# Performance work log

Hardware: AMD Instinct MI355X
Metric: run time of the kernel (lower is better)

The kernel has to match this reference:

```python
import jax, jax.numpy as jnp
import numpy as np

# bitsandbytes NF4 codebook (16 levels)
NF4 = jnp.array([-1.0, -0.6961928009986877, -0.5250730514526367, -0.39491748809814453,
                 -0.28444138169288635, -0.18477343022823334, -0.09105003625154495, 0.0,
                 0.07958029955625534, 0.16093020141124725, 0.24611230194568634,
                 0.33791524171829224, 0.44070982933044434, 0.5626170039176941,
                 0.7229568362236023, 1.0], dtype=jnp.float32)
BLOCK = 64  # NF4 quantization blocksize
HD, M, TOKENS = 4096, 11008, 512


def dequant_nf4(codes, absmax, out_f, in_f):
    # codes: int [out_f, in_f] in [0,16); absmax: float [out_f*in_f/BLOCK]
    w = NF4[codes.reshape(-1, BLOCK)] * absmax[:, None]
    return w.reshape(out_f, in_f)


def setup_inputs() -> dict:
    key = jax.random.key(0)
    ks = jax.random.split(key, 7)
    x = jax.random.normal(ks[0], (TOKENS, HD), dtype=jnp.float32)
    gate_codes = jax.random.randint(ks[1], (M, HD), 0, 16, dtype=jnp.int32)
    up_codes = jax.random.randint(ks[2], (M, HD), 0, 16, dtype=jnp.int32)
    down_codes = jax.random.randint(ks[3], (HD, M), 0, 16, dtype=jnp.int32)
    n_blk = (M * HD) // BLOCK
    gate_absmax = jax.random.uniform(ks[4], (n_blk,), dtype=jnp.float32) * 0.02 + 1e-3
    up_absmax = jax.random.uniform(ks[5], (n_blk,), dtype=jnp.float32) * 0.02 + 1e-3
    down_absmax = jax.random.uniform(ks[6], (n_blk,), dtype=jnp.float32) * 0.02 + 1e-3
    return {"x": x, "gate_codes": gate_codes, "gate_absmax": gate_absmax,
            "up_codes": up_codes, "up_absmax": up_absmax,
            "down_codes": down_codes, "down_absmax": down_absmax}


def reference(x, gate_codes, gate_absmax, up_codes, up_absmax, down_codes, down_absmax):
    # Dequantize NF4 weights on the fly, then SwiGLU MLP:
    # down( silu(gate(x)) * up(x) )
    Wg = dequant_nf4(gate_codes, gate_absmax, M, HD)   # [m, hd]
    Wu = dequant_nf4(up_codes, up_absmax, M, HD)       # [m, hd]
    Wd = dequant_nf4(down_codes, down_absmax, HD, M)   # [hd, m]
    g = x @ Wg.T                                       # [tokens, m]
    u = x @ Wu.T                                       # [tokens, m]
    h = jax.nn.silu(g) * u                             # [tokens, m]
    return h @ Wd.T                                    # [tokens, hd]
```

## Files before the change

### kernel.cpp

```cpp
#include <hip/hip_runtime.h>
#include <hip/hip_fp16.h>
#include <cstdint>
#include <cstddef>


using float4v = __attribute__((ext_vector_type(4))) float;
using half8   = __attribute__((ext_vector_type(8))) _Float16;

__constant__ float NF4TAB[16] = {
  -1.0f, -0.6961928009986877f, -0.5250730514526367f, -0.39491748809814453f,
  -0.28444138169288635f, -0.18477343022823334f, -0.09105003625154495f, 0.0f,
  0.07958029955625534f, 0.16093020141124725f, 0.24611230194568634f,
  0.33791524171829224f, 0.44070982933044434f, 0.5626170039176941f,
  0.7229568362236023f, 1.0f };


__global__ __launch_bounds__(256) void repack_kernel(
    const int* __restrict__ codes, const float* __restrict__ amax,
    unsigned char* __restrict__ outp, float* __restrict__ outam,
    int K, int Kb, int KbG)
{
  __shared__ unsigned char lds[4][32 * 36];
  const int tid  = threadIdx.x;
  const int lane = tid & 63;
  const int w    = tid >> 6;
  const int l15  = lane & 15;
  const int hi   = lane >> 4;

  const int bid  = blockIdx.x;
  const int tile = bid / KbG;
  const int kb   = (bid % KbG) * 4 + w;

  const int* src = codes + (size_t)tile * 32 * K + (size_t)kb * 64;

  #pragma unroll
  for (int i = 0; i < 8; ++i) {
    const int row = i * 4 + hi;
    const int4 c = *(const int4*)(src + (size_t)row * K + l15 * 4);
    const unsigned short v =
      (unsigned short)((c.x | (c.y << 4)) | ((c.z | (c.w << 4)) << 8));
    *(unsigned short*)&lds[w][row * 36 + l15 * 2] = v;
  }
  asm volatile("s_waitcnt lgkmcnt(0)" ::: "memory");
  __builtin_amdgcn_sched_barrier(0);

  uint4 o;
  o.x = *(const unsigned*)&lds[w][l15 * 36 + hi * 4];
  o.y = *(const unsigned*)&lds[w][l15 * 36 + 16 + hi * 4];
  o.z = *(const unsigned*)&lds[w][(l15 + 16) * 36 + hi * 4];
  o.w = *(const unsigned*)&lds[w][(l15 + 16) * 36 + 16 + hi * 4];
  *(uint4*)(outp + (((size_t)tile * Kb + kb) * 64 + lane) * 16) = o;

  if (lane < 32)
    outam[((size_t)tile * Kb + kb) * 32 + lane] =
      amax[(size_t)(tile * 32 + lane) * Kb + kb];
}

template <bool ATOMIC>
__global__ __launch_bounds__(256, 3) void gemm_nf4(
    const __half* __restrict__ Apk,
    const unsigned char* __restrict__ p0, const float* __restrict__ am0,
    const unsigned char* __restrict__ p1, const float* __restrict__ am1,
    __half* __restrict__ o0, __half* __restrict__ o1,
    float* __restrict__ outF,
    int N, int K, int Kc, int Ntiles)
{
  __shared__ unsigned ptab[256];

  const int tid  = threadIdx.x;
  const int lane = tid & 63;
  const int wave = tid >> 6;
  const int l15  = lane & 15;

  {
    __half2 pr = __floats2half2_rn(NF4TAB[tid & 15], NF4TAB[tid >> 4]);
    ptab[tid] = *(const unsigned*)&pr;
  }
  __syncthreads();

  int nt, r2;
  if (ATOMIC) {
    const int xcd  = blockIdx.x & 7;
    const int slot = blockIdx.x >> 3;
    r2 = xcd >> 1;
    nt = (xcd & 1) * (Ntiles >> 1) + slot;
  } else {
    const int nwg = gridDim.x;
    const int bid = (blockIdx.x & 7) * (nwg >> 3) + (blockIdx.x >> 3);
    nt = bid % Ntiles;
    r2 = bid / Ntiles;
  }

  const int k0 = ATOMIC ? r2 * Kc : 0;
  const int nk = Kc >> 6;
  const unsigned char* pk = (!ATOMIC && r2) ? p1 : p0;
  const float* amx        = (!ATOMIC && r2) ? am1 : am0;
  __half* outH            = (!ATOMIC && r2) ? o1 : o0;

  const int col0 = nt * 32;
  const int Kb   = K >> 6;
  const int kb0q = k0 >> 6;

  const uint4* pc  = (const uint4*)(pk + (((size_t)nt * Kb + kb0q) * 64 + lane) * 16);
  const float* pam = amx + ((size_t)nt * Kb + kb0q) * 32 + l15;

  const __half* pA = Apk + ((size_t)((k0 >> 5) * 32 + wave * 8)) * 512
                         + (size_t)lane * 8;

  float4v acc[8][2];
  {
    float4v z = {0.f, 0.f, 0.f, 0.f};
    #pragma unroll
    for (int i = 0; i < 8; ++i)
      #pragma unroll
      for (int j = 0; j < 2; ++j) acc[i][j] = z;
  }

  uint4 cq;
  float af[2];

#define LOADCQ()                                                                \
  { cq = *pc; af[0] = pam[0]; af[1] = pam[16];                                  \
    pc += 64; pam += 32; }

#define DEQD(DST, D, AM2)                                                       \
  { unsigned _w0 = ptab[(D) & 255];                                             \
    unsigned _w1 = ptab[((D) >> 8) & 255];                                      \
    unsigned _w2 = ptab[((D) >> 16) & 255];                                     \
    unsigned _w3 = ptab[(D) >> 24];                                             \
    __half2 _p0 = __hmul2(*(const __half2*)&_w0, AM2);                          \
    __half2 _p1 = __hmul2(*(const __half2*)&_w1, AM2);                          \
    __half2 _p2 = __hmul2(*(const __half2*)&_w2, AM2);                          \
    __half2 _p3 = __hmul2(*(const __half2*)&_w3, AM2);                          \
    uint4 _wv;                                                                  \
    _wv.x = *(const unsigned*)&_p0; _wv.y = *(const unsigned*)&_p1;             \
    _wv.z = *(const unsigned*)&_p2; _wv.w = *(const unsigned*)&_p3;             \
    DST = *(const half8*)&_wv; }

  LOADCQ();

  for (int kt = 0; kt < nk; ++kt) {
    const __half _a0 = __float2half(af[0]);
    const __half _a1 = __float2half(af[1]);
    const __half2 am20{_a0, _a0}, am21{_a1, _a1};
    half8 bq00, bq01, bq10, bq11;
    DEQD(bq00, cq.x, am20);
    DEQD(bq01, cq.y, am20);
    DEQD(bq10, cq.z, am21);
    DEQD(bq11, cq.w, am21);

    half8 ap[8];
    #pragma unroll
    for (int i = 0; i < 8; ++i)
      ap[i] = *(const half8*)(pA + i * 512);

    if (kt + 1 < nk) LOADCQ();

    #pragma unroll
    for (int i = 0; i < 8; ++i) {
      acc[i][0] = __builtin_amdgcn_mfma_f32_16x16x32_f16(ap[i], bq00, acc[i][0], 0, 0, 0);
      acc[i][1] = __builtin_amdgcn_mfma_f32_16x16x32_f16(ap[i], bq10, acc[i][1], 0, 0, 0);
    }

    #pragma unroll
    for (int i = 0; i < 8; ++i)
      ap[i] = *(const half8*)(pA + 16384 + i * 512);

    #pragma unroll
    for (int i = 0; i < 8; ++i) {
      acc[i][0] = __builtin_amdgcn_mfma_f32_16x16x32_f16(ap[i], bq01, acc[i][0], 0, 0, 0);
      acc[i][1] = __builtin_amdgcn_mfma_f32_16x16x32_f16(ap[i], bq11, acc[i][1], 0, 0, 0);
    }

    pA += 32768;
  }

  if (ATOMIC) {
    const int ccol0 = col0 + l15;
    const int crow0 = wave * 128 + ((lane >> 4) << 2);
    #pragma unroll
    for (int i = 0; i < 8; ++i)
      #pragma unroll
      for (int j = 0; j < 2; ++j)
        #pragma unroll
        for (int rr = 0; rr < 4; ++rr) {
          const size_t idx = (size_t)(crow0 + i * 16 + rr) * N + (ccol0 + j * 16);
          atomicAdd(&outF[idx], acc[i][j][rr]);
        }
  } else {
    const int jj    = lane & 7;
    const int lb    = (lane >> 3) & 1;
    const int rbase = (lane >> 4) << 2;
    const int kb    = col0 >> 5;
    #pragma unroll
    for (int i = 0; i < 8; ++i) {
      const int mb = wave * 8 + i;
      #pragma unroll
      for (int j = 0; j < 2; ++j) {
        const int lp = (j * 2 + lb) * 16 + rbase;
        #pragma unroll
        for (int rr = 0; rr < 4; ++rr) {
          const size_t a = ((size_t)(kb * 32 + mb) * 64 + (lp + rr)) * 8 + jj;
          outH[a] = __float2half(acc[i][j][rr]);
        }
      }
    }
  }
#undef LOADCQ
#undef DEQD
}

__global__ void cast_pack_kernel(const float* __restrict__ x,
                                 __half* __restrict__ xp, int nGrp) {
  int pid = blockIdx.x * blockDim.x + threadIdx.x;
  if (pid >= nGrp) return;
  const int lane = pid & 63;
  const int grp  = pid >> 6;
  const int mb   = grp & 31;
  const int kb   = grp >> 5;
  const int m = mb * 16 + (lane & 15);
  const int k = kb * 32 + ((lane >> 4) << 3);
  const float4* src = (const float4*)(x + (size_t)m * 4096 + k);
  float4 v0 = src[0], v1 = src[1];
  __half2 h0 = __floats2half2_rn(v0.x, v0.y), h1 = __floats2half2_rn(v0.z, v0.w);
  __half2 h2 = __floats2half2_rn(v1.x, v1.y), h3 = __floats2half2_rn(v1.z, v1.w);
  uint4 o;
  o.x = *(const unsigned*)&h0; o.y = *(const unsigned*)&h1;
  o.z = *(const unsigned*)&h2; o.w = *(const unsigned*)&h3;
  ((uint4*)xp)[pid] = o;
}

__global__ void swiglu_kernel(const __half* __restrict__ g,
                              const __half* __restrict__ u,
                              __half* __restrict__ h, int n2) {
  int i = blockIdx.x * blockDim.x + threadIdx.x;
  if (i < n2) {
    float2 gf = __half22float2(((const __half2*)g)[i]);
    float2 uf = __half22float2(((const __half2*)u)[i]);
    float h0 = gf.x / (1.f + __expf(-gf.x)) * uf.x;
    float h1 = gf.y / (1.f + __expf(-gf.y)) * uf.y;
    ((__half2*)h)[i] = __floats2half2_rn(h0, h1);
  }
}

extern "C" void kernel_launch(void* const* d_in, const int* in_sizes, int n_in,
                              void* d_out, int out_size, void* d_ws, size_t ws_size,
                              hipStream_t stream)
{
  (void)in_sizes; (void)n_in; (void)ws_size;
  const float* x            = (const float*)d_in[0];
  const int*   gate_codes   = (const int*)d_in[1];
  const float* gate_absmax  = (const float*)d_in[2];
  const int*   up_codes     = (const int*)d_in[3];
  const float* up_absmax    = (const float*)d_in[4];
  const int*   down_codes   = (const int*)d_in[5];
  const float* down_absmax  = (const float*)d_in[6];
  float* out = (float*)d_out;

  __half* xp = (__half*)d_ws;
  __half* g  = xp + (size_t)512 * 4096;
  __half* u  = g  + (size_t)512 * 11008;
  unsigned char* pg = (unsigned char*)(u + (size_t)512 * 11008);
  unsigned char* pu = pg + (size_t)344 * 64 * 1024;
  unsigned char* pd = pu + (size_t)344 * 64 * 1024;
  float* amg = (float*)(pd + (size_t)128 * 172 * 1024);
  float* amu = amg + (size_t)344 * 64 * 32;
  float* amd = amu + (size_t)344 * 64 * 32;

  hipMemsetAsync(d_out, 0, (size_t)out_size * sizeof(float), stream);

  cast_pack_kernel<<<1024, 256, 0, stream>>>(x, xp, (512 * 4096) / 8);

  repack_kernel<<<5504, 256, 0, stream>>>(gate_codes, gate_absmax, pg, amg,
                                          4096, 64, 16);
  repack_kernel<<<5504, 256, 0, stream>>>(up_codes, up_absmax, pu, amu,
                                          4096, 64, 16);
  repack_kernel<<<5504, 256, 0, stream>>>(down_codes, down_absmax, pd, amd,
                                          11008, 172, 43);

  gemm_nf4<false><<<688, 256, 0, stream>>>(xp, pg, amg, pu, amu,
                                           g, u, nullptr,
                                           11008, 4096, 4096, 344);

  swiglu_kernel<<<11008, 256, 0, stream>>>(g, u, g, (512 * 11008) / 2);

  gemm_nf4<true><<<512, 256, 0, stream>>>(g, pd, amd,
                                          nullptr, nullptr, nullptr, nullptr,
                                          out, 4096, 11008, 2752, 128);
}
```

Measured before the change: 810.9 us.

## Reshape NF4 GEMM tiles to 256x64 with 4x4 MFMA blocking and double-buffered codes

The GEMM workgroup tile changes from 512 rows by 32 columns to 256 rows by 64 columns. Each wave now holds a 4x4 grid of MFMA accumulators, so every A fragment is reused across four dequantized B fragments and fewer A loads are needed per MFMA. The repack kernel now writes a 64-column packed layout directly from registers with no LDS staging. The main loop is unrolled by two, with separate prefetch registers for the codes and absmax two steps ahead. In exchange, more dequantization work is done per wave for each A load, and register pressure may rise under the launch bound of 3.

New measurement: 705.3 us. 1.15x faster.

```diff
diff --git a/kernel.cpp b/kernel.cpp
--- a/kernel.cpp
+++ b/kernel.cpp
@@ -17,43 +17,47 @@
 
 __global__ __launch_bounds__(256) void repack_kernel(
     const int* __restrict__ codes, const float* __restrict__ amax,
-    unsigned char* __restrict__ outp, float* __restrict__ outam,
+    unsigned char* __restrict__ pb, float* __restrict__ pam,
     int K, int Kb, int KbG)
 {
-  __shared__ unsigned char lds[4][32 * 36];
   const int tid  = threadIdx.x;
   const int lane = tid & 63;
   const int w    = tid >> 6;
   const int l15  = lane & 15;
   const int hi   = lane >> 4;
 
-  const int bid  = blockIdx.x;
-  const int tile = bid / KbG;
-  const int kb   = (bid % KbG) * 4 + w;
-
-  const int* src = codes + (size_t)tile * 32 * K + (size_t)kb * 64;
-
+  const int tile = blockIdx.x / KbG;
+  const int kbg  = blockIdx.x % KbG;
+  const int kb   = kbg * 4 + w;
+
+  unsigned dk0[4], dk1[4];
   #pragma unroll
-  for (int i = 0; i < 8; ++i) {
-    const int row = i * 4 + hi;
-    const int4 c = *(const int4*)(src + (size_t)row * K + l15 * 4);
-    const unsigned short v =
-      (unsigned short)((c.x | (c.y << 4)) | ((c.z | (c.w << 4)) << 8));
-    *(unsigned short*)&lds[w][row * 36 + l15 * 2] = v;
-  }
-  asm volatile("s_waitcnt lgkmcnt(0)" ::: "memory");
-  __builtin_amdgcn_sched_barrier(0);
-
-  uint4 o;
-  o.x = *(const unsigned*)&lds[w][l15 * 36 + hi * 4];
-  o.y = *(const unsigned*)&lds[w][l15 * 36 + 16 + hi * 4];
-  o.z = *(const unsigned*)&lds[w][(l15 + 16) * 36 + hi * 4];
-  o.w = *(const unsigned*)&lds[w][(l15 + 16) * 36 + 16 + hi * 4];
-  *(uint4*)(outp + (((size_t)tile * Kb + kb) * 64 + lane) * 16) = o;
-
-  if (lane < 32)
-    outam[((size_t)tile * Kb + kb) * 32 + lane] =
-      amax[(size_t)(tile * 32 + lane) * Kb + kb];
+  for (int j = 0; j < 4; ++j) {
+    const int* base = codes + (size_t)(tile * 64 + j * 16 + l15) * K
+                            + (size_t)kb * 64;
+    const int4 a0 = *(const int4*)(base + hi * 8);
+    const int4 a1 = *(const int4*)(base + hi * 8 + 4);
+    const int4 b0 = *(const int4*)(base + 32 + hi * 8);
+    const int4 b1 = *(const int4*)(base + 32 + hi * 8 + 4);
+    dk0[j] = (unsigned)((a0.x | (a0.y << 4)) | ((a0.z | (a0.w << 4)) << 8) |
+                        ((a1.x | (a1.y << 4)) << 16) | ((a1.z | (a1.w << 4)) << 24));
+    dk1[j] = (unsigned)((b0.x | (b0.y << 4)) | ((b0.z | (b0.w << 4)) << 8) |
+                        ((b1.x | (b1.y << 4)) << 16) | ((b1.z | (b1.w << 4)) << 24));
+  }
+  uint4 o0, o1;
+  o0.x = dk0[0]; o0.y = dk1[0]; o0.z = dk0[1]; o0.w = dk1[1];
+  o1.x = dk0[2]; o1.y = dk1[2]; o1.z = dk0[3]; o1.w = dk1[3];
+  uint4* dst = (uint4*)(pb + (((size_t)tile * Kb + kb) * 64 + lane) * 32);
+  dst[0] = o0; dst[1] = o1;
+
+  if (w == 0) {
+    const float4 am = *(const float4*)(amax + (size_t)(tile * 64 + lane) * Kb
+                                            + kbg * 4);
+    pam[((size_t)tile * Kb + kbg * 4 + 0) * 64 + lane] = am.x;
+    pam[((size_t)tile * Kb + kbg * 4 + 1) * 64 + lane] = am.y;
+    pam[((size_t)tile * Kb + kbg * 4 + 2) * 64 + lane] = am.z;
+    pam[((size_t)tile * Kb + kbg * 4 + 3) * 64 + lane] = am.w;
+  }
 }
 
 template <bool ATOMIC>
@@ -78,17 +82,20 @@
   }
   __syncthreads();
 
-  int nt, r2;
+  int nt, r2, mt;
   if (ATOMIC) {
     const int xcd  = blockIdx.x & 7;
     const int slot = blockIdx.x >> 3;
     r2 = xcd >> 1;
-    nt = (xcd & 1) * (Ntiles >> 1) + slot;
+    mt = slot & 1;
+    nt = (slot >> 1) + (xcd & 1) * 32;
   } else {
     const int nwg = gridDim.x;
     const int bid = (blockIdx.x & 7) * (nwg >> 3) + (blockIdx.x >> 3);
-    nt = bid % Ntiles;
-    r2 = bid / Ntiles;
+    mt = bid & 1;
+    const int r = bid >> 1;
+    nt = r % Ntiles;
+    r2 = r / Ntiles;
   }
 
   const int k0 = ATOMIC ? r2 * Kc : 0;
@@ -97,31 +104,39 @@
   const float* amx        = (!ATOMIC && r2) ? am1 : am0;
   __half* outH            = (!ATOMIC && r2) ? o1 : o0;
 
-  const int col0 = nt * 32;
+  const int col0 = nt * 64;
   const int Kb   = K >> 6;
   const int kb0q = k0 >> 6;
 
-  const uint4* pc  = (const uint4*)(pk + (((size_t)nt * Kb + kb0q) * 64 + lane) * 16);
-  const float* pam = amx + ((size_t)nt * Kb + kb0q) * 32 + l15;
-
-  const __half* pA = Apk + ((size_t)((k0 >> 5) * 32 + wave * 8)) * 512
+  const uint4* pc  = (const uint4*)(pk + (((size_t)nt * Kb + kb0q) * 64 + lane) * 32);
+  const float* pam = amx + ((size_t)nt * Kb + kb0q) * 64 + l15;
+
+  const int mb0 = mt * 16 + wave * 4;
+  const __half* pA = Apk + ((size_t)((k0 >> 5) * 32 + mb0) * 512)
                          + (size_t)lane * 8;
 
-  float4v acc[8][2];
+  float4v acc[4][4];
   {
     float4v z = {0.f, 0.f, 0.f, 0.f};
     #pragma unroll
-    for (int i = 0; i < 8; ++i)
+    for (int i = 0; i < 4; ++i)
       #pragma unroll
-      for (int j = 0; j < 2; ++j) acc[i][j] = z;
-  }
-
-  uint4 cq;
-  float af[2];
-
-#define LOADCQ()                                                                \
-  { cq = *pc; af[0] = pam[0]; af[1] = pam[16];                                  \
-    pc += 64; pam += 32; }
+      for (int j = 0; j < 4; ++j) acc[i][j] = z;
+  }
+
+  uint4 q0_0, q1_0, q0_1, q1_1;
+  float af_0[4], af_1[4];
+
+#define LOADCQ0(KT)                                                             \
+  { const uint4* _p = pc + (size_t)(KT) * 128;                                  \
+    q0_0 = _p[0]; q1_0 = _p[1];                                                 \
+    const float* _a = pam + (size_t)(KT) * 64;                                  \
+    af_0[0] = _a[0]; af_0[1] = _a[16]; af_0[2] = _a[32]; af_0[3] = _a[48]; }
+#define LOADCQ1(KT)                                                             \
+  { const uint4* _p = pc + (size_t)(KT) * 128;                                  \
+    q0_1 = _p[0]; q1_1 = _p[1];                                                 \
+    const float* _a = pam + (size_t)(KT) * 64;                                  \
+    af_1[0] = _a[0]; af_1[1] = _a[16]; af_1[2] = _a[32]; af_1[3] = _a[48]; }
 
 #define DEQD(DST, D, AM2)                                                       \
   { unsigned _w0 = ptab[(D) & 255];                                             \
@@ -137,51 +152,50 @@
     _wv.z = *(const unsigned*)&_p2; _wv.w = *(const unsigned*)&_p3;             \
     DST = *(const half8*)&_wv; }
 
-  LOADCQ();
-
-  for (int kt = 0; kt < nk; ++kt) {
-    const __half _a0 = __float2half(af[0]);
-    const __half _a1 = __float2half(af[1]);
-    const __half2 am20{_a0, _a0}, am21{_a1, _a1};
-    half8 bq00, bq01, bq10, bq11;
-    DEQD(bq00, cq.x, am20);
-    DEQD(bq01, cq.y, am20);
-    DEQD(bq10, cq.z, am21);
-    DEQD(bq11, cq.w, am21);
-
-    half8 ap[8];
-    #pragma unroll
-    for (int i = 0; i < 8; ++i)
-      ap[i] = *(const half8*)(pA + i * 512);
-
-    if (kt + 1 < nk) LOADCQ();
-
-    #pragma unroll
-    for (int i = 0; i < 8; ++i) {
-      acc[i][0] = __builtin_amdgcn_mfma_f32_16x16x32_f16(ap[i], bq00, acc[i][0], 0, 0, 0);
-      acc[i][1] = __builtin_amdgcn_mfma_f32_16x16x32_f16(ap[i], bq10, acc[i][1], 0, 0, 0);
-    }
-
-    #pragma unroll
-    for (int i = 0; i < 8; ++i)
-      ap[i] = *(const half8*)(pA + 16384 + i * 512);
-
-    #pragma unroll
-    for (int i = 0; i < 8; ++i) {
-      acc[i][0] = __builtin_amdgcn_mfma_f32_16x16x32_f16(ap[i], bq01, acc[i][0], 0, 0, 0);
-      acc[i][1] = __builtin_amdgcn_mfma_f32_16x16x32_f16(ap[i], bq11, acc[i][1], 0, 0, 0);
-    }
-
-    pA += 32768;
-  }
+#define BODY(KT, S)                                                             \
+  { half8 bq[4], ap[4];                                                         \
+    { const __half _a0 = __float2half(af_##S[0]);                               \
+      const __half _a1 = __float2half(af_##S[1]);                               \
+      const __half _a2 = __float2half(af_##S[2]);                               \
+      const __half _a3 = __float2half(af_##S[3]);                               \
+      const __half2 _m0{_a0,_a0}, _m1{_a1,_a1}, _m2{_a2,_a2}, _m3{_a3,_a3};     \
+      DEQD(bq[0], q0_##S.x, _m0); DEQD(bq[1], q0_##S.z, _m1);                   \
+      DEQD(bq[2], q1_##S.x, _m2); DEQD(bq[3], q1_##S.z, _m3);                   \
+      _Pragma("unroll")                                                         \
+      for (int _i = 0; _i < 4; ++_i)                                            \
+        ap[_i] = *(const half8*)(pA + (size_t)(KT) * 32768 + _i * 512);         \
+      _Pragma("unroll")                                                         \
+      for (int _i = 0; _i < 4; ++_i)                                            \
+        _Pragma("unroll")                                                       \
+        for (int _j = 0; _j < 4; ++_j)                                          \
+          acc[_i][_j] = __builtin_amdgcn_mfma_f32_16x16x32_f16(ap[_i], bq[_j], acc[_i][_j], 0, 0, 0); \
+      DEQD(bq[0], q0_##S.y, _m0); DEQD(bq[1], q0_##S.w, _m1);                   \
+      DEQD(bq[2], q1_##S.y, _m2); DEQD(bq[3], q1_##S.w, _m3);                   \
+      _Pragma("unroll")                                                         \
+      for (int _i = 0; _i < 4; ++_i)                                            \
+        ap[_i] = *(const half8*)(pA + (size_t)(KT) * 32768 + 16384 + _i * 512); \
+      _Pragma("unroll")                                                         \
+      for (int _i = 0; _i < 4; ++_i)                                            \
+        _Pragma("unroll")                                                       \
+        for (int _j = 0; _j < 4; ++_j)                                          \
+          acc[_i][_j] = __builtin_amdgcn_mfma_f32_16x16x32_f16(ap[_i], bq[_j], acc[_i][_j], 0, 0, 0); \
+    }                                                                           \
+    if ((KT) + 2 < nk) { LOADCQ##S((KT) + 2); } }
+
+  LOADCQ0(0);
+  if (nk > 1) LOADCQ1(1);
+
+  int kt = 0;
+  while (kt + 2 <= nk) { BODY(kt, 0); BODY(kt + 1, 1); kt += 2; }
+  if (kt < nk) BODY(kt, 0);
 
   if (ATOMIC) {
     const int ccol0 = col0 + l15;
-    const int crow0 = wave * 128 + ((lane >> 4) << 2);
+    const int crow0 = mt * 256 + wave * 64 + ((lane >> 4) << 2);
     #pragma unroll
-    for (int i = 0; i < 8; ++i)
+    for (int i = 0; i < 4; ++i)
       #pragma unroll
-      for (int j = 0; j < 2; ++j)
+      for (int j = 0; j < 4; ++j)
         #pragma unroll
         for (int rr = 0; rr < 4; ++rr) {
           const size_t idx = (size_t)(crow0 + i * 16 + rr) * N + (ccol0 + j * 16);
@@ -191,13 +205,13 @@
     const int jj    = lane & 7;
     const int lb    = (lane >> 3) & 1;
     const int rbase = (lane >> 4) << 2;
-    const int kb    = col0 >> 5;
     #pragma unroll
-    for (int i = 0; i < 8; ++i) {
-      const int mb = wave * 8 + i;
+    for (int i = 0; i < 4; ++i) {
+      const int mb = mb0 + i;
       #pragma unroll
-      for (int j = 0; j < 2; ++j) {
-        const int lp = (j * 2 + lb) * 16 + rbase;
+      for (int j = 0; j < 4; ++j) {
+        const int kb = nt * 2 + (j >> 1);
+        const int lp = ((j & 1) * 2 + lb) * 16 + rbase;
         #pragma unroll
         for (int rr = 0; rr < 4; ++rr) {
           const size_t a = ((size_t)(kb * 32 + mb) * 64 + (lp + rr)) * 8 + jj;
@@ -206,8 +220,10 @@
       }
     }
   }
-#undef LOADCQ
+#undef LOADCQ0
+#undef LOADCQ1
 #undef DEQD
+#undef BODY
 }
 
 __global__ void cast_pack_kernel(const float* __restrict__ x,
@@ -261,30 +277,30 @@
   __half* g  = xp + (size_t)512 * 4096;
   __half* u  = g  + (size_t)512 * 11008;
   unsigned char* pg = (unsigned char*)(u + (size_t)512 * 11008);
-  unsigned char* pu = pg + (size_t)344 * 64 * 1024;
-  unsigned char* pd = pu + (size_t)344 * 64 * 1024;
-  float* amg = (float*)(pd + (size_t)128 * 172 * 1024);
-  float* amu = amg + (size_t)344 * 64 * 32;
-  float* amd = amu + (size_t)344 * 64 * 32;
+  unsigned char* pu = pg + (size_t)172 * 64 * 2048;
+  unsigned char* pd = pu + (size_t)172 * 64 * 2048;
+  float* amg = (float*)(pd + (size_t)64 * 172 * 2048);
+  float* amu = amg + (size_t)172 * 64 * 64;
+  float* amd = amu + (size_t)172 * 64 * 64;
 
   hipMemsetAsync(d_out, 0, (size_t)out_size * sizeof(float), stream);
 
   cast_pack_kernel<<<1024, 256, 0, stream>>>(x, xp, (512 * 4096) / 8);
 
-  repack_kernel<<<5504, 256, 0, stream>>>(gate_codes, gate_absmax, pg, amg,
+  repack_kernel<<<2752, 256, 0, stream>>>(gate_codes, gate_absmax, pg, amg,
                                           4096, 64, 16);
-  repack_kernel<<<5504, 256, 0, stream>>>(up_codes, up_absmax, pu, amu,
+  repack_kernel<<<2752, 256, 0, stream>>>(up_codes, up_absmax, pu, amu,
                                           4096, 64, 16);
-  repack_kernel<<<5504, 256, 0, stream>>>(down_codes, down_absmax, pd, amd,
+  repack_kernel<<<2752, 256, 0, stream>>>(down_codes, down_absmax, pd, amd,
                                           11008, 172, 43);
 
   gemm_nf4<false><<<688, 256, 0, stream>>>(xp, pg, amg, pu, amu,
                                            g, u, nullptr,
-                                           11008, 4096, 4096, 344);
+                                           11008, 4096, 4096, 172);
 
   swiglu_kernel<<<11008, 256, 0, stream>>>(g, u, g, (512 * 11008) / 2);
 
   gemm_nf4<true><<<512, 256, 0, stream>>>(g, pd, amd,
                                           nullptr, nullptr, nullptr, nullptr,
-                                          out, 4096, 11008, 2752, 128);
-}
+                                          out, 4096, 11008, 2752, 64);
+}
```
